# Optimization experiments

Measured on AMD Instinct MI355X. Metric: run time of the kernel, lower is better.

## Reference

```python
import jax, jax.numpy as jnp
import numpy as np

NEG_INF = -1000000000.0
INPUT_SIZE = 1024
HIDDEN_SIZE = 64
B, S = 8, 2048


def setup_inputs() -> dict:
    key = jax.random.key(0)
    ks = jax.random.split(key, 8)
    scale = 1.0 / np.sqrt(INPUT_SIZE)
    inp = {
        "input": jax.random.normal(ks[0], (B, S, INPUT_SIZE), dtype=jnp.float32),
        "mask": jax.random.randint(ks[1], (B, S, S), 0, 2, dtype=jnp.int32),
        "W_q": jax.random.uniform(ks[2], (HIDDEN_SIZE, INPUT_SIZE), jnp.float32, -scale, scale),
        "b_q": jax.random.uniform(ks[3], (HIDDEN_SIZE,), jnp.float32, -scale, scale),
        "W_k": jax.random.uniform(ks[4], (HIDDEN_SIZE, INPUT_SIZE), jnp.float32, -scale, scale),
        "b_k": jax.random.uniform(ks[5], (HIDDEN_SIZE,), jnp.float32, -scale, scale),
        "W_v": jax.random.uniform(ks[6], (HIDDEN_SIZE, INPUT_SIZE), jnp.float32, -scale, scale),
        "b_v": jax.random.uniform(ks[7], (HIDDEN_SIZE,), jnp.float32, -scale, scale),
    }
    return inp


def reference(input, mask, W_q, b_q, W_k, b_k, W_v, b_v):
    inv_sqrt_d = 1.0 / np.sqrt(HIDDEN_SIZE)
    # Q/K/V projections: torch Linear is x @ W.T + b
    q = jnp.einsum('bsi,hi->bsh', input, W_q) + b_q  # (B,S,H)
    k = jnp.einsum('bsi,hi->bsh', input, W_k) + b_k
    v = jnp.einsum('bsi,hi->bsh', input, W_v) + b_v
    scores = jnp.einsum('bqh,bkh->bqk', q, k) * inv_sqrt_d  # (B,S,S)
    scores = jnp.where(mask == 0, NEG_INF, scores)
    probs = jax.nn.softmax(scores, axis=-1)
    return jnp.einsum('bqk,bkh->bqh', probs, v)  # (B,S,H)
```

## Files before the change

### kernel.cpp

```cpp
#include <hip/hip_runtime.h>

typedef __bf16 bf16;
typedef bf16 bf16x4 __attribute__((ext_vector_type(4)));
typedef bf16 bf16x8 __attribute__((ext_vector_type(8)));
typedef float floatx4 __attribute__((ext_vector_type(4)));
typedef unsigned int u32;
typedef unsigned long long u64;

#define B_ 8
#define S_ 2048
#define I_ 1024
#define H_ 64

__global__ void conv_w(const float* __restrict__ Wq, const float* __restrict__ bq,
                       const float* __restrict__ Wk, const float* __restrict__ bk,
                       const float* __restrict__ Wv, const float* __restrict__ bv,
                       bf16* __restrict__ Wf, float* __restrict__ bc) {
    int idx = blockIdx.x * 256 + threadIdx.x;
    int nrow = idx >> 10, i = idx & 1023;
    float v;
    if (nrow < 64)       v = Wq[nrow * I_ + i] * 0.125f;
    else if (nrow < 128) v = Wk[(nrow - 64) * I_ + i];
    else                 v = Wv[(nrow - 128) * I_ + i];
    int kc = i >> 5, t = i & 31, g = t >> 3, j = t & 7;
    int nt = nrow >> 4, nl = nrow & 15;
    Wf[(size_t)(kc * 12 + nt) * 512 + (g * 16 + nl) * 8 + j] = (bf16)v;
    if (idx < 192) {
        float bb = (idx < 64) ? bq[idx] * 0.125f
                 : (idx < 128) ? bk[idx - 64] : bv[idx - 128];
        bc[idx] = bb;
    }
}

__global__ __launch_bounds__(64) void qkv_gemm(const float* __restrict__ X,
                                               const bf16* __restrict__ Wf,
                                               const float* __restrict__ bc,
                                               bf16* __restrict__ Qd,
                                               bf16* __restrict__ Kd2,
                                               bf16* __restrict__ Vt2) {
    __shared__ __align__(16) bf16 Xs[16 * 136];

    int lane = threadIdx.x;
    int n = lane & 15, g = lane >> 4;
    int m0 = blockIdx.x * 16;

    floatx4 zero4 = {0.0f, 0.0f, 0.0f, 0.0f};
    floatx4 acc[12];
#pragma unroll
    for (int t = 0; t < 12; ++t) acc[t] = zero4;

    const float* xb = X + (size_t)m0 * I_;

    float4 xr[8];
#pragma unroll
    for (int q = 0; q < 8; ++q) {
        int f = q * 256 + lane * 4;
        xr[q] = *(const float4*)(xb + (size_t)(f >> 7) * I_ + (f & 127));
    }

    for (int s = 0; s < 8; ++s) {
#pragma unroll
        for (int q = 0; q < 8; ++q) {
            int f = q * 256 + lane * 4;
            bf16x4 xv;
            xv[0] = (bf16)xr[q].x; xv[1] = (bf16)xr[q].y;
            xv[2] = (bf16)xr[q].z; xv[3] = (bf16)xr[q].w;
            *(bf16x4*)(Xs + (f >> 7) * 136 + (f & 127)) = xv;
        }
        if (s < 7) {
#pragma unroll
            for (int q = 0; q < 8; ++q) {
                int f = q * 256 + lane * 4;
                xr[q] = *(const float4*)(xb + (size_t)(f >> 7) * I_ + (s + 1) * 128 + (f & 127));
            }
        }
#pragma unroll
        for (int ks = 0; ks < 4; ++ks) {
            bf16x8 xa = *(bf16x8*)(Xs + n * 136 + ks * 32 + g * 8);
            const bf16* wrow = Wf + (size_t)((s * 4 + ks) * 12) * 512 + lane * 8;
#pragma unroll
            for (int nt = 0; nt < 12; ++nt) {
                bf16x8 wb = *(const bf16x8*)(wrow + nt * 512);
                acc[nt] = __builtin_amdgcn_mfma_f32_16x16x32_bf16(xa, wb, acc[nt], 0, 0, 0);
            }
        }
    }

    int b = m0 >> 11;
    int sb = (m0 & 2047) + g * 4;
#pragma unroll
    for (int nt = 0; nt < 12; ++nt) {
        int ng = nt * 16 + n;
        float bias = bc[ng];
        if (ng < 64) {
#pragma unroll
            for (int r = 0; r < 4; ++r)
                Qd[(size_t)(b * S_ + sb + r) * H_ + ng] = (bf16)(acc[nt][r] + bias);
        } else if (ng < 128) {
            int hc = (ng - 64) >> 3, j = (ng - 64) & 7;
#pragma unroll
            for (int r = 0; r < 4; ++r)
                Kd2[((size_t)(b * 8 + hc) * S_ + sb + r) * 8 + j] = (bf16)(acc[nt][r] + bias);
        } else {
            int hh = ng - 128, kc = sb >> 3, jj = sb & 7;
            bf16x4 pk;
#pragma unroll
            for (int r = 0; r < 4; ++r) pk[r] = (bf16)(acc[nt][r] + bias);
            *(bf16x4*)(Vt2 + ((size_t)(b * 256 + kc) * 64 + hh) * 8 + jj) = pk;
        }
    }
}

__global__ __launch_bounds__(256, 2) void attn(const bf16* __restrict__ Qd,
                                               const bf16* __restrict__ Kd2,
                                               const bf16* __restrict__ Vt2,
                                               const int* __restrict__ mask,
                                               float* __restrict__ po,
                                               float* __restrict__ pl) {
    __shared__ __align__(16) bf16 Ps[64 * 136];

    int tid = threadIdx.x;
    int w = tid >> 6, lane = tid & 63;
    int n = lane & 15, g = lane >> 4;
    int bid = blockIdx.x;
    int ksp = bid & 3;
    int qt = (bid >> 2) & 31;
    int b = bid >> 7;
    int q0 = qt * 64;

    const bf16* qptr = Qd + (size_t)(b * S_ + q0 + w * 16 + n) * H_ + g * 8;
    bf16x8 qa0 = *(const bf16x8*)qptr;
    bf16x8 qa1 = *(const bf16x8*)(qptr + 32);

    floatx4 zero4 = {0.0f, 0.0f, 0.0f, 0.0f};
    floatx4 o[4];
#pragma unroll
    for (int t = 0; t < 4; ++t) o[t] = zero4;
    float l_i[4] = {0.0f, 0.0f, 0.0f, 0.0f};

    const int* msl = mask + (size_t)(b * S_ + q0 + w * 16) * S_ + lane;
    const bf16* kp0 = Kd2 + (size_t)(b * 8 + g) * S_ * 8;
    const bf16* kp1 = Kd2 + (size_t)(b * 8 + 4 + g) * S_ * 8;
    const bf16* vp  = Vt2 + (size_t)(b * 256) * 512;

    for (int kt = ksp * 4; kt < ksp * 4 + 4; ++kt) {
        int mv[16][2];
#pragma unroll
        for (int rr = 0; rr < 16; ++rr)
#pragma unroll
            for (int c = 0; c < 2; ++c)
                mv[rr][c] = msl[(size_t)rr * S_ + kt * 128 + c * 64];

        floatx4 s[8];
#pragma unroll
        for (int nt = 0; nt < 8; ++nt) {
            bf16x8 k0 = *(const bf16x8*)(kp0 + (size_t)(kt * 128 + nt * 16 + n) * 8);
            bf16x8 k1 = *(const bf16x8*)(kp1 + (size_t)(kt * 128 + nt * 16 + n) * 8);
            floatx4 a = zero4;
            a = __builtin_amdgcn_mfma_f32_16x16x32_bf16(qa0, k0, a, 0, 0, 0);
            a = __builtin_amdgcn_mfma_f32_16x16x32_bf16(qa1, k1, a, 0, 0, 0);
            s[nt] = a;
        }

        u64 bal0[16], bal1[16];
#pragma unroll
        for (int rr = 0; rr < 16; ++rr) {
            bal0[rr] = __ballot(mv[rr][0] != 0);
            bal1[rr] = __ballot(mv[rr][1] != 0);
        }
        u32 mq[4][4];
#pragma unroll
        for (int r = 0; r < 4; ++r) {
            u64 s0 = (g == 0) ? bal0[r] : (g == 1) ? bal0[4 + r]
                   : (g == 2) ? bal0[8 + r] : bal0[12 + r];
            u64 s1 = (g == 0) ? bal1[r] : (g == 1) ? bal1[4 + r]
                   : (g == 2) ? bal1[8 + r] : bal1[12 + r];
            mq[r][0] = (u32)s0; mq[r][1] = (u32)(s0 >> 32);
            mq[r][2] = (u32)s1; mq[r][3] = (u32)(s1 >> 32);
        }

#pragma unroll
        for (int r = 0; r < 4; ++r)
#pragma unroll
            for (int nt = 0; nt < 8; ++nt) {
                float e = __expf(s[nt][r]);
                bool bit = (mq[r][nt >> 1] >> ((nt & 1) * 16 + n)) & 1u;
                float p = bit ? e : 0.0f;
                s[nt][r] = p;
                l_i[r] += p;
            }

#pragma unroll
        for (int r = 0; r < 4; ++r)
#pragma unroll
            for (int nt = 0; nt < 8; ++nt)
                Ps[(w * 16 + g * 4 + r) * 136 + nt * 16 + n] = (bf16)s[nt][r];

#pragma unroll
        for (int k0 = 0; k0 < 4; ++k0) {
            bf16x8 pa = *(bf16x8*)(Ps + (w * 16 + n) * 136 + k0 * 32 + g * 8);
#pragma unroll
            for (int ht = 0; ht < 4; ++ht) {
                bf16x8 vb = *(const bf16x8*)(vp +
                    ((size_t)(kt * 16 + k0 * 4 + g) * 64 + ht * 16 + n) * 8);
                o[ht] = __builtin_amdgcn_mfma_f32_16x16x32_bf16(pa, vb, o[ht], 0, 0, 0);
            }
        }
    }

#pragma unroll
    for (int r = 0; r < 4; ++r)
#pragma unroll
        for (int off = 1; off < 16; off <<= 1)
            l_i[r] += __shfl_xor(l_i[r], off, 64);

    float* pb = po + (size_t)bid * 4096;
#pragma unroll
    for (int ht = 0; ht < 4; ++ht)
#pragma unroll
        for (int r = 0; r < 4; ++r)
            pb[(w * 16 + g * 4 + r) * 64 + ht * 16 + n] = o[ht][r];
    if (n == 0) {
#pragma unroll
        for (int r = 0; r < 4; ++r)
            pl[(size_t)bid * 64 + w * 16 + g * 4 + r] = l_i[r];
    }
}

__global__ __launch_bounds__(256) void reduce_o(const float* __restrict__ po,
                                                const float* __restrict__ pl,
                                                float* __restrict__ out) {
    int idx = blockIdx.x * 256 + threadIdx.x;
    int h = idx & 63, q = idx >> 6;
    int b = q >> 11, qq = q & 2047;
    int qt = qq >> 6, ql = qq & 63;
    int bid0 = (b * 32 + qt) * 4;
    float num = 0.0f, den = 0.0f;
#pragma unroll
    for (int j = 0; j < 4; ++j) {
        den += pl[(size_t)(bid0 + j) * 64 + ql];
        num += po[(size_t)(bid0 + j) * 4096 + ql * 64 + h];
    }
    out[(size_t)q * 64 + h] = num / den;
}

extern "C" void kernel_launch(void* const* d_in, const int* in_sizes, int n_in,
                              void* d_out, int out_size, void* d_ws, size_t ws_size,
                              hipStream_t stream) {
    const float* X    = (const float*)d_in[0];
    const int*   mask = (const int*)d_in[1];
    const float* Wq   = (const float*)d_in[2];
    const float* bq   = (const float*)d_in[3];
    const float* Wk   = (const float*)d_in[4];
    const float* bk   = (const float*)d_in[5];
    const float* Wv   = (const float*)d_in[6];
    const float* bv   = (const float*)d_in[7];
    float* out = (float*)d_out;

    char* p = (char*)d_ws;
    bf16* Qd   = (bf16*)p;  p += (size_t)B_ * S_ * H_ * 2;
    bf16* Kd2  = (bf16*)p;  p += (size_t)B_ * S_ * H_ * 2;
    bf16* Vt2  = (bf16*)p;  p += (size_t)B_ * S_ * H_ * 2;
    bf16* Wf   = (bf16*)p;  p += (size_t)192 * 1024 * 2;
    float* bc  = (float*)p; p += 1024;
    float* po  = (float*)p; p += (size_t)1024 * 4096 * 4;
    float* pl  = (float*)p; p += (size_t)1024 * 64 * 4;

    conv_w<<<dim3(768), dim3(256), 0, stream>>>(Wq, bq, Wk, bk, Wv, bv, Wf, bc);
    qkv_gemm<<<dim3(1024), dim3(64), 0, stream>>>(X, Wf, bc, Qd, Kd2, Vt2);
    attn<<<dim3(1024), dim3(256), 0, stream>>>(Qd, Kd2, Vt2, mask, po, pl);
    reduce_o<<<dim3(4096), dim3(256), 0, stream>>>(po, pl, out);
}
```

Measured before the change: 278.3 us.

## Split QKV GEMM across 4 waves, double attention key splits, stage K via async LDS

The QKV projection now runs 256-thread blocks. The whole 16x1024 X tile is converted into LDS once, and each wave computes 3 of the 12 output column tiles, which raises occupancy. Attention splits the key range 8 ways instead of 4, giving 2048 blocks. K chunks are staged into shared memory with global_load_lds async copies, and the mask is loaded directly in the MFMA layout instead of using ballots. The cost is extra block-level barriers, twice as many partial results for the reduction kernel to combine, and a shared LDS buffer reused for both K and P.

```diff
diff --git a/kernel.cpp b/kernel.cpp
--- a/kernel.cpp
+++ b/kernel.cpp
@@ -5,12 +5,17 @@
 typedef bf16 bf16x8 __attribute__((ext_vector_type(8)));
 typedef float floatx4 __attribute__((ext_vector_type(4)));
 typedef unsigned int u32;
-typedef unsigned long long u64;
 
 #define B_ 8
 #define S_ 2048
 #define I_ 1024
 #define H_ 64
+
+__device__ __forceinline__ void async_cp16(bf16* lds_base, const bf16* g_base, int lane) {
+    __builtin_amdgcn_global_load_lds(
+        (const __attribute__((address_space(1))) u32*)(g_base + lane * 8),
+        (__attribute__((address_space(3))) u32*)lds_base, 16, 0, 0);
+}
 
 __global__ void conv_w(const float* __restrict__ Wq, const float* __restrict__ bq,
                        const float* __restrict__ Wk, const float* __restrict__ bk,
@@ -32,65 +37,54 @@
     }
 }
 
-__global__ __launch_bounds__(64) void qkv_gemm(const float* __restrict__ X,
-                                               const bf16* __restrict__ Wf,
-                                               const float* __restrict__ bc,
-                                               bf16* __restrict__ Qd,
-                                               bf16* __restrict__ Kd2,
-                                               bf16* __restrict__ Vt2) {
-    __shared__ __align__(16) bf16 Xs[16 * 136];
-
-    int lane = threadIdx.x;
+__global__ __launch_bounds__(256, 4) void qkv_gemm(const float* __restrict__ X,
+                                                   const bf16* __restrict__ Wf,
+                                                   const float* __restrict__ bc,
+                                                   bf16* __restrict__ Qd,
+                                                   bf16* __restrict__ Kd2,
+                                                   bf16* __restrict__ Vt2) {
+    __shared__ __align__(16) bf16 Xs[16 * 1032];
+
+    int tid = threadIdx.x;
+    int w = tid >> 6, lane = tid & 63;
     int n = lane & 15, g = lane >> 4;
     int m0 = blockIdx.x * 16;
 
     floatx4 zero4 = {0.0f, 0.0f, 0.0f, 0.0f};
-    floatx4 acc[12];
-#pragma unroll
-    for (int t = 0; t < 12; ++t) acc[t] = zero4;
-
-    const float* xb = X + (size_t)m0 * I_;
-
-    float4 xr[8];
-#pragma unroll
-    for (int q = 0; q < 8; ++q) {
-        int f = q * 256 + lane * 4;
-        xr[q] = *(const float4*)(xb + (size_t)(f >> 7) * I_ + (f & 127));
-    }
-
-    for (int s = 0; s < 8; ++s) {
-#pragma unroll
-        for (int q = 0; q < 8; ++q) {
-            int f = q * 256 + lane * 4;
-            bf16x4 xv;
-            xv[0] = (bf16)xr[q].x; xv[1] = (bf16)xr[q].y;
-            xv[2] = (bf16)xr[q].z; xv[3] = (bf16)xr[q].w;
-            *(bf16x4*)(Xs + (f >> 7) * 136 + (f & 127)) = xv;
-        }
-        if (s < 7) {
-#pragma unroll
-            for (int q = 0; q < 8; ++q) {
-                int f = q * 256 + lane * 4;
-                xr[q] = *(const float4*)(xb + (size_t)(f >> 7) * I_ + (s + 1) * 128 + (f & 127));
-            }
-        }
-#pragma unroll
-        for (int ks = 0; ks < 4; ++ks) {
-            bf16x8 xa = *(bf16x8*)(Xs + n * 136 + ks * 32 + g * 8);
-            const bf16* wrow = Wf + (size_t)((s * 4 + ks) * 12) * 512 + lane * 8;
-#pragma unroll
-            for (int nt = 0; nt < 12; ++nt) {
-                bf16x8 wb = *(const bf16x8*)(wrow + nt * 512);
-                acc[nt] = __builtin_amdgcn_mfma_f32_16x16x32_bf16(xa, wb, acc[nt], 0, 0, 0);
-            }
+    floatx4 acc[3];
+#pragma unroll
+    for (int t = 0; t < 3; ++t) acc[t] = zero4;
+
+    {
+        int row = tid >> 4, cb = (tid & 15) * 4;
+        const float* xr = X + (size_t)(m0 + row) * I_ + cb;
+        bf16* xd = Xs + row * 1032 + cb;
+#pragma unroll
+        for (int q = 0; q < 16; ++q) {
+            float4 v = *(const float4*)(xr + q * 64);
+            bf16x4 xb;
+            xb[0] = (bf16)v.x; xb[1] = (bf16)v.y; xb[2] = (bf16)v.z; xb[3] = (bf16)v.w;
+            *(bf16x4*)(xd + q * 64) = xb;
+        }
+    }
+    __syncthreads();
+
+    const bf16* wl = Wf + (size_t)(w * 3) * 512 + lane * 8;
+    for (int ks = 0; ks < 32; ++ks) {
+        bf16x8 xa = *(bf16x8*)(Xs + n * 1032 + ks * 32 + g * 8);
+        const bf16* wrow = wl + (size_t)ks * 12 * 512;
+#pragma unroll
+        for (int nt = 0; nt < 3; ++nt) {
+            bf16x8 wb = *(const bf16x8*)(wrow + nt * 512);
+            acc[nt] = __builtin_amdgcn_mfma_f32_16x16x32_bf16(xa, wb, acc[nt], 0, 0, 0);
         }
     }
 
     int b = m0 >> 11;
     int sb = (m0 & 2047) + g * 4;
 #pragma unroll
-    for (int nt = 0; nt < 12; ++nt) {
-        int ng = nt * 16 + n;
+    for (int nt = 0; nt < 3; ++nt) {
+        int ng = w * 48 + nt * 16 + n;
         float bias = bc[ng];
         if (ng < 64) {
 #pragma unroll
@@ -111,21 +105,21 @@
     }
 }
 
-__global__ __launch_bounds__(256, 2) void attn(const bf16* __restrict__ Qd,
+__global__ __launch_bounds__(256, 6) void attn(const bf16* __restrict__ Qd,
                                                const bf16* __restrict__ Kd2,
                                                const bf16* __restrict__ Vt2,
                                                const int* __restrict__ mask,
                                                float* __restrict__ po,
                                                float* __restrict__ pl) {
-    __shared__ __align__(16) bf16 Ps[64 * 136];
+    __shared__ __align__(16) bf16 regA[8704];
 
     int tid = threadIdx.x;
     int w = tid >> 6, lane = tid & 63;
     int n = lane & 15, g = lane >> 4;
     int bid = blockIdx.x;
-    int ksp = bid & 3;
-    int qt = (bid >> 2) & 31;
-    int b = bid >> 7;
+    int ksp = bid & 7;
+    int qt = (bid >> 3) & 31;
+    int b = bid >> 8;
     int q0 = qt * 64;
 
     const bf16* qptr = Qd + (size_t)(b * S_ + q0 + w * 16 + n) * H_ + g * 8;
@@ -138,45 +132,35 @@
     for (int t = 0; t < 4; ++t) o[t] = zero4;
     float l_i[4] = {0.0f, 0.0f, 0.0f, 0.0f};
 
-    const int* msl = mask + (size_t)(b * S_ + q0 + w * 16) * S_ + lane;
-    const bf16* kp0 = Kd2 + (size_t)(b * 8 + g) * S_ * 8;
-    const bf16* kp1 = Kd2 + (size_t)(b * 8 + 4 + g) * S_ * 8;
-    const bf16* vp  = Vt2 + (size_t)(b * 256) * 512;
-
-    for (int kt = ksp * 4; kt < ksp * 4 + 4; ++kt) {
-        int mv[16][2];
-#pragma unroll
-        for (int rr = 0; rr < 16; ++rr)
-#pragma unroll
-            for (int c = 0; c < 2; ++c)
-                mv[rr][c] = msl[(size_t)rr * S_ + kt * 128 + c * 64];
+    const bf16* vp = Vt2 + (size_t)(b * 256) * 512;
+
+    for (int kt = ksp * 2; kt < ksp * 2 + 2; ++kt) {
+        const int* mb = mask + (size_t)(b * S_ + q0 + w * 16 + g * 4) * S_ + kt * 128 + n;
+        int mreg[4][8];
+#pragma unroll
+        for (int r = 0; r < 4; ++r)
+#pragma unroll
+            for (int nt = 0; nt < 8; ++nt)
+                mreg[r][nt] = mb[(size_t)r * S_ + nt * 16];
+#pragma unroll
+        for (int j = 0; j < 2; ++j) {
+            int hc = w * 2 + j;
+#pragma unroll
+            for (int p = 0; p < 2; ++p)
+                async_cp16(regA + hc * 1040 + p * 512,
+                           Kd2 + ((size_t)(b * 8 + hc) * S_ + kt * 128 + p * 64) * 8, lane);
+        }
+        __syncthreads();
 
         floatx4 s[8];
 #pragma unroll
         for (int nt = 0; nt < 8; ++nt) {
-            bf16x8 k0 = *(const bf16x8*)(kp0 + (size_t)(kt * 128 + nt * 16 + n) * 8);
-            bf16x8 k1 = *(const bf16x8*)(kp1 + (size_t)(kt * 128 + nt * 16 + n) * 8);
             floatx4 a = zero4;
-            a = __builtin_amdgcn_mfma_f32_16x16x32_bf16(qa0, k0, a, 0, 0, 0);
-            a = __builtin_amdgcn_mfma_f32_16x16x32_bf16(qa1, k1, a, 0, 0, 0);
+            a = __builtin_amdgcn_mfma_f32_16x16x32_bf16(
+                    qa0, *(const bf16x8*)(regA + g * 1040 + (nt * 16 + n) * 8), a, 0, 0, 0);
+            a = __builtin_amdgcn_mfma_f32_16x16x32_bf16(
+                    qa1, *(const bf16x8*)(regA + (4 + g) * 1040 + (nt * 16 + n) * 8), a, 0, 0, 0);
             s[nt] = a;
-        }
-
-        u64 bal0[16], bal1[16];
-#pragma unroll
-        for (int rr = 0; rr < 16; ++rr) {
-            bal0[rr] = __ballot(mv[rr][0] != 0);
-            bal1[rr] = __ballot(mv[rr][1] != 0);
-        }
-        u32 mq[4][4];
-#pragma unroll
-        for (int r = 0; r < 4; ++r) {
-            u64 s0 = (g == 0) ? bal0[r] : (g == 1) ? bal0[4 + r]
-                   : (g == 2) ? bal0[8 + r] : bal0[12 + r];
-            u64 s1 = (g == 0) ? bal1[r] : (g == 1) ? bal1[4 + r]
-                   : (g == 2) ? bal1[8 + r] : bal1[12 + r];
-            mq[r][0] = (u32)s0; mq[r][1] = (u32)(s0 >> 32);
-            mq[r][2] = (u32)s1; mq[r][3] = (u32)(s1 >> 32);
         }
 
 #pragma unroll
@@ -184,21 +168,22 @@
 #pragma unroll
             for (int nt = 0; nt < 8; ++nt) {
                 float e = __expf(s[nt][r]);
-                bool bit = (mq[r][nt >> 1] >> ((nt & 1) * 16 + n)) & 1u;
-                float p = bit ? e : 0.0f;
+                float p = (mreg[r][nt] != 0) ? e : 0.0f;
                 s[nt][r] = p;
                 l_i[r] += p;
             }
+        __syncthreads();
 
 #pragma unroll
         for (int r = 0; r < 4; ++r)
 #pragma unroll
             for (int nt = 0; nt < 8; ++nt)
-                Ps[(w * 16 + g * 4 + r) * 136 + nt * 16 + n] = (bf16)s[nt][r];
+                regA[(w * 16 + g * 4 + r) * 136 + nt * 16 + n] = (bf16)s[nt][r];
+        __syncthreads();
 
 #pragma unroll
         for (int k0 = 0; k0 < 4; ++k0) {
-            bf16x8 pa = *(bf16x8*)(Ps + (w * 16 + n) * 136 + k0 * 32 + g * 8);
+            bf16x8 pa = *(bf16x8*)(regA + (w * 16 + n) * 136 + k0 * 32 + g * 8);
 #pragma unroll
             for (int ht = 0; ht < 4; ++ht) {
                 bf16x8 vb = *(const bf16x8*)(vp +
@@ -206,6 +191,7 @@
                 o[ht] = __builtin_amdgcn_mfma_f32_16x16x32_bf16(pa, vb, o[ht], 0, 0, 0);
             }
         }
+        __syncthreads();
     }
 
 #pragma unroll
@@ -234,10 +220,10 @@
     int h = idx & 63, q = idx >> 6;
     int b = q >> 11, qq = q & 2047;
     int qt = qq >> 6, ql = qq & 63;
-    int bid0 = (b * 32 + qt) * 4;
+    int bid0 = (b * 32 + qt) * 8;
     float num = 0.0f, den = 0.0f;
 #pragma unroll
-    for (int j = 0; j < 4; ++j) {
+    for (int j = 0; j < 8; ++j) {
         den += pl[(size_t)(bid0 + j) * 64 + ql];
         num += po[(size_t)(bid0 + j) * 4096 + ql * 64 + h];
     }
@@ -263,11 +249,11 @@
     bf16* Vt2  = (bf16*)p;  p += (size_t)B_ * S_ * H_ * 2;
     bf16* Wf   = (bf16*)p;  p += (size_t)192 * 1024 * 2;
     float* bc  = (float*)p; p += 1024;
-    float* po  = (float*)p; p += (size_t)1024 * 4096 * 4;
-    float* pl  = (float*)p; p += (size_t)1024 * 64 * 4;
+    float* po  = (float*)p; p += (size_t)2048 * 4096 * 4;
+    float* pl  = (float*)p; p += (size_t)2048 * 64 * 4;
 
     conv_w<<<dim3(768), dim3(256), 0, stream>>>(Wq, bq, Wk, bk, Wv, bv, Wf, bc);
-    qkv_gemm<<<dim3(1024), dim3(64), 0, stream>>>(X, Wf, bc, Qd, Kd2, Vt2);
-    attn<<<dim3(1024), dim3(256), 0, stream>>>(Qd, Kd2, Vt2, mask, po, pl);
+    qkv_gemm<<<dim3(1024), dim3(256), 0, stream>>>(X, Wf, bc, Qd, Kd2, Vt2);
+    attn<<<dim3(2048), dim3(256), 0, stream>>>(Qd, Kd2, Vt2, mask, po, pl);
     reduce_o<<<dim3(4096), dim3(256), 0, stream>>>(po, pl, out);
 }
```

New measurement: 322.8 us. +16.0%, slower.
